# Optimization experiments

Measured on AMD Instinct MI355X. Metric: run time of the kernel, lower is better.

Reference implementation:

```python
import jax, jax.numpy as jnp
import numpy as np

V, F, H, P, C = 50000, 300, 256, 128, 10   # vocab, emb dim, n_hid, n_penultimate, n_class
B, S, N = 128, 16, 64                      # docs, sentences/doc, word nodes/sentence (last = master)
G, T = B * S, B * S * N                    # sentence graphs, total word nodes
EPS = 1e-5


def _mp(h, adj, w1, b1, w2, b2):
    # MessagePassing: neighborhood aggregation (block-diag spmm) + 2-layer ReLU MLP
    m = jnp.einsum('gij,gjf->gif', adj, h)
    return jax.nn.relu(jax.nn.relu(m @ w1 + b1) @ w2 + b2)


def _att(h, w, b, v, use_master):
    # Attention readout: alpha = softmax(relu(hW+b)v) over nodes, weighted sum;
    # with master node, last node is split off and concatenated to the pooled vector.
    if use_master:
        t, h = h[:, -1, :], h[:, :-1, :]
    logits = jnp.einsum('gnh,h->gn', jax.nn.relu(h @ w + b), v)
    alpha = jax.nn.softmax(logits, axis=1)
    pooled = jnp.einsum('gn,gnh->gh', alpha, h)
    return jnp.concatenate([pooled, t], axis=1) if use_master else pooled


def setup_inputs():
    key = jax.random.key(0)
    ks = iter(jax.random.split(key, 40))
    def nrm(shape, s=0.05):
        return jax.random.normal(next(ks), shape, jnp.float32) * s
    x = jax.random.randint(next(ks), (T,), 0, V)
    adj = jax.random.uniform(next(ks), (G, N, N), jnp.float32)
    adj = adj / jnp.sum(adj, -1, keepdims=True)         # row-normalized word-graph blocks
    adj_s = jax.random.uniform(next(ks), (B, S, S), jnp.float32)
    adj_s = adj_s / jnp.sum(adj_s, -1, keepdims=True)   # sentence-graph blocks (unused in sentence_att branch)
    return dict(
        x=x, adj=adj, adj_s=adj_s, shape0=N, shape1=S,
        emb=nrm((V, F), 0.1),
        mp0_w1=nrm((F, H)), mp0_b1=jnp.zeros((H,)), mp0_w2=nrm((H, H)), mp0_b2=jnp.zeros((H,)),
        mp1_w1=nrm((H, H)), mp1_b1=jnp.zeros((H,)), mp1_w2=nrm((H, H)), mp1_b2=jnp.zeros((H,)),
        att0_w=nrm((H, H)), att0_b=jnp.zeros((H,)), att0_v=nrm((H,)),
        att1_w=nrm((H, H)), att1_b=jnp.zeros((H,)), att1_v=nrm((H,)),
        bn_gamma=jnp.ones((4 * H,)), bn_beta=jnp.zeros((4 * H,)),
        fc1_w=nrm((4 * H, H)), fc1_b=jnp.zeros((H,)),
        satt_w=nrm((H, H)), satt_b=jnp.zeros((H,)), satt_v=nrm((H,)),
        fc2_w=nrm((H, P)), fc2_b=jnp.zeros((P,)),
        fc3_w=nrm((P, C)), fc3_b=jnp.zeros((C,)),
    )


def reference(x, adj, adj_s, shape0, shape1, emb,
              mp0_w1, mp0_b1, mp0_w2, mp0_b2,
              mp1_w1, mp1_b1, mp1_w2, mp1_b2,
              att0_w, att0_b, att0_v, att1_w, att1_b, att1_v,
              bn_gamma, bn_beta, fc1_w, fc1_b,
              satt_w, satt_b, satt_v, fc2_w, fc2_b, fc3_w, fc3_b):
    h = emb[x].reshape(-1, shape0, emb.shape[1])        # [G, N, F] (dropout is identity at eval)
    reps = []
    for (w1, b1, w2, b2, aw, ab, av) in (
            (mp0_w1, mp0_b1, mp0_w2, mp0_b2, att0_w, att0_b, att0_v),
            (mp1_w1, mp1_b1, mp1_w2, mp1_b2, att1_w, att1_b, att1_v)):
        h = _mp(h, adj, w1, b1, w2, b2)                  # [G, N, H]
        reps.append(_att(h, aw, ab, av, True))           # [G, 2H]
    z = jnp.concatenate(reps, axis=1)                    # [G, 2*n_mp*H] = [G, 4H]
    mu, var = jnp.mean(z, 0), jnp.var(z, 0)              # BatchNorm1d (batch statistics)
    z = (z - mu) / jnp.sqrt(var + EPS) * bn_gamma + bn_beta
    z = jax.nn.relu(z @ fc1_w + fc1_b)                   # [G, H]
    z = z.reshape(-1, shape1, z.shape[1])                # [B, S, H]
    z = _att(z, satt_w, satt_b, satt_v, False)           # sentence attention -> [B, H]
    z = jax.nn.relu(z @ fc2_w + fc2_b)                   # [B, P]
    z = z @ fc3_w + fc3_b                                # [B, C]
    return jax.nn.log_softmax(z, axis=1)
```

## Files before the change

kernel.cpp:

```cpp
#include <hip/hip_runtime.h>
#include <math.h>


typedef unsigned short u16;
typedef __attribute__((ext_vector_type(8))) short bf16x8;
typedef __attribute__((ext_vector_type(4))) float f32x4;

__device__ __forceinline__ float b2f(u16 v){ return __uint_as_float(((unsigned)v)<<16); }
__device__ __forceinline__ u16 f2b(float f){
    unsigned u = __float_as_uint(f);
    return (u16)((u + 0x7FFFu + ((u>>16)&1u)) >> 16);
}
__device__ __forceinline__ ushort4 pack4(float a,float b,float c,float d){
    ushort4 o; o.x=f2b(a); o.y=f2b(b); o.z=f2b(c); o.w=f2b(d); return o;
}

#define SCOL_OFF 32768
__device__ __forceinline__ int srow_b(int nd, int f){
    return (nd*512 + f*2) ^ ((nd&7)<<4);
}
__device__ __forceinline__ int scol_b(int f, int nd){
    return SCOL_OFF + ((f*128 + nd*2) ^ ((f&7)<<4));
}

__global__ __launch_bounds__(512, 2) void mega_k(
    const int* __restrict__ x, const u16* __restrict__ adjb,
    const u16* __restrict__ eprime,
    const u16* __restrict__ wb_w2a, const u16* __restrict__ wb_awa,
    const u16* __restrict__ wb_w1b, const u16* __restrict__ wb_w2b,
    const u16* __restrict__ wb_awb,
    const float* __restrict__ b1a, const float* __restrict__ b2a,
    const float* __restrict__ aba, const float* __restrict__ ava,
    const float* __restrict__ b1b, const float* __restrict__ b2b,
    const float* __restrict__ abb, const float* __restrict__ avb,
    u16* __restrict__ zb)
{
    __shared__ __align__(16) char sm[65536];
    const int g = blockIdx.x, tid = threadIdx.x;
    const int w = tid>>6, l = tid&63, lgp = l>>4, ll = l&15;
    const f32x4 zero4 = {0.f,0.f,0.f,0.f};

    {
        const int r2 = tid >> 3;
        const int fc = (tid & 7) * 32;
        const u16* ep = eprime + (long)x[g*64 + r2]*256 + fc;
        uint4 q0 = *(const uint4*)(ep);
        uint4 q1 = *(const uint4*)(ep + 8);
        uint4 q2 = *(const uint4*)(ep + 16);
        uint4 q3 = *(const uint4*)(ep + 24);
        #pragma unroll
        for (int qi=0; qi<4; ++qi){
            uint4 v = (qi==0)?q0:(qi==1)?q1:(qi==2)?q2:q3;
            unsigned xw[4] = {v.x, v.y, v.z, v.w};
            #pragma unroll
            for (int wi=0; wi<4; ++wi){
                unsigned u = xw[wi];
                int f0 = fc + qi*8 + wi*2;
                *(u16*)(sm + scol_b(f0,   r2)) = (u16)(u & 0xffffu);
                *(u16*)(sm + scol_b(f0+1, r2)) = (u16)(u >> 16);
            }
        }
        __syncthreads();
    }

    const u16* adjbg = adjb + (long)g*4096;

    #pragma unroll 1
    for (int layer=0; layer<2; ++layer){
        const u16* wb_w2 = layer ? wb_w2b : wb_w2a;
        const u16* wb_aw = layer ? wb_awb : wb_awa;
        const float* b1  = layer ? b1b : b1a;
        const float* b2  = layer ? b2b : b2a;
        const float* ab  = layer ? abb : aba;
        const float* av  = layer ? avb : ava;
        const int zoff   = layer ? 512 : 0;

        {
            f32x4 acc[2][4];
            #pragma unroll
            for (int j=0;j<4;++j){ acc[0][j] = zero4; acc[1][j] = zero4; }
            #pragma unroll
            for (int t=0;t<2;++t){
                const int k0 = t*32 + lgp*8;
                bf16x8 a0 = *(const bf16x8*)(sm + scol_b(w*32 +      ll, k0));
                bf16x8 a1 = *(const bf16x8*)(sm + scol_b(w*32 + 16 + ll, k0));
                bf16x8 b[4];
                #pragma unroll
                for (int ni=0;ni<4;++ni)
                    b[ni] = *(const bf16x8*)(adjbg + (ni*16+ll)*64 + k0);
                #pragma unroll
                for (int ni=0;ni<4;++ni){
                    acc[0][ni] = __builtin_amdgcn_mfma_f32_16x16x32_bf16(a0, b[ni], acc[0][ni],0,0,0);
                    acc[1][ni] = __builtin_amdgcn_mfma_f32_16x16x32_bf16(a1, b[ni], acc[1][ni],0,0,0);
                }
            }
            #pragma unroll
            for (int mi=0;mi<2;++mi){
                int f0 = w*32 + mi*16 + lgp*4;
                float4 bi = *(const float4*)(b1 + f0);
                #pragma unroll
                for (int ni=0;ni<4;++ni){
                    int nd = ni*16 + ll;
                    f32x4 v = acc[mi][ni];
                    *(ushort4*)(sm + srow_b(nd, f0)) = pack4(
                        fmaxf(v[0]+bi.x,0.f), fmaxf(v[1]+bi.y,0.f),
                        fmaxf(v[2]+bi.z,0.f), fmaxf(v[3]+bi.w,0.f));
                }
            }
            __syncthreads();
        }

        {
            f32x4 acc[2][4];
            #pragma unroll
            for (int j=0;j<4;++j){ acc[0][j] = zero4; acc[1][j] = zero4; }
            const u16* chw = wb_w2 + (w<<10) + ll*32 + lgp*8;
            bf16x8 w0 = *(const bf16x8*)(chw);
            bf16x8 w1 = *(const bf16x8*)(chw + 512);
            #pragma unroll
            for (int t=0;t<8;++t){
                bf16x8 cw0 = w0, cw1 = w1;
                if (t < 7){
                    const u16* nx = chw + (t+1)*8192;
                    w0 = *(const bf16x8*)(nx);
                    w1 = *(const bf16x8*)(nx + 512);
                }
                const int k0 = t*32 + lgp*8;
                bf16x8 b[4];
                #pragma unroll
                for (int ni=0;ni<4;++ni) b[ni] = *(const bf16x8*)(sm + srow_b(ni*16+ll, k0));
                #pragma unroll
                for (int ni=0;ni<4;++ni){
                    acc[0][ni] = __builtin_amdgcn_mfma_f32_16x16x32_bf16(cw0, b[ni], acc[0][ni],0,0,0);
                    acc[1][ni] = __builtin_amdgcn_mfma_f32_16x16x32_bf16(cw1, b[ni], acc[1][ni],0,0,0);
                }
            }
            __syncthreads();
            #pragma unroll
            for (int mi=0;mi<2;++mi){
                int f0 = w*32 + mi*16 + lgp*4;
                float4 bi = *(const float4*)(b2 + f0);
                #pragma unroll
                for (int ni=0;ni<4;++ni){
                    int nd = ni*16 + ll;
                    f32x4 v = acc[mi][ni];
                    *(ushort4*)(sm + srow_b(nd, f0)) = pack4(
                        fmaxf(v[0]+bi.x,0.f), fmaxf(v[1]+bi.y,0.f),
                        fmaxf(v[2]+bi.z,0.f), fmaxf(v[3]+bi.w,0.f));
                }
            }
            __syncthreads();
        }

        {
            f32x4 acc[4][2];
            #pragma unroll
            for (int i=0;i<4;++i){ acc[i][0] = zero4; acc[i][1] = zero4; }
            const u16* chw = wb_aw + (w<<10) + ll*32 + lgp*8;
            bf16x8 w0 = *(const bf16x8*)(chw);
            bf16x8 w1 = *(const bf16x8*)(chw + 512);
            #pragma unroll
            for (int t=0;t<8;++t){
                bf16x8 cw0 = w0, cw1 = w1;
                if (t < 7){
                    const u16* nx = chw + (t+1)*8192;
                    w0 = *(const bf16x8*)(nx);
                    w1 = *(const bf16x8*)(nx + 512);
                }
                const int k0 = t*32 + lgp*8;
                bf16x8 a[4];
                #pragma unroll
                for (int mi=0;mi<4;++mi) a[mi] = *(const bf16x8*)(sm + srow_b(mi*16+ll, k0));
                #pragma unroll
                for (int mi=0;mi<4;++mi){
                    acc[mi][0] = __builtin_amdgcn_mfma_f32_16x16x32_bf16(a[mi], cw0, acc[mi][0],0,0,0);
                    acc[mi][1] = __builtin_amdgcn_mfma_f32_16x16x32_bf16(a[mi], cw1, acc[mi][1],0,0,0);
                }
            }
            float abv[2], avv[2];
            #pragma unroll
            for (int ni=0;ni<2;++ni){ abv[ni] = ab[w*32+ni*16+ll]; avv[ni] = av[w*32+ni*16+ll]; }
            float lgt[4][4];
            #pragma unroll
            for (int mi=0;mi<4;++mi){
                #pragma unroll
                for (int r=0;r<4;++r) lgt[mi][r] = 0.f;
            }
            #pragma unroll
            for (int mi=0;mi<4;++mi){
                #pragma unroll
                for (int ni=0;ni<2;++ni){
                    f32x4 v = acc[mi][ni];
                    #pragma unroll
                    for (int r=0;r<4;++r) lgt[mi][r] += fmaxf(v[r]+abv[ni],0.f)*avv[ni];
                }
            }
            #pragma unroll
            for (int mi=0;mi<4;++mi){
                #pragma unroll
                for (int r=0;r<4;++r){
                    float vv = lgt[mi][r];
                    vv += __shfl_xor(vv,1,64); vv += __shfl_xor(vv,2,64);
                    vv += __shfl_xor(vv,4,64); vv += __shfl_xor(vv,8,64);
                    lgt[mi][r] = vv;
                }
            }
            float* red   = (float*)(sm + SCOL_OFF);
            float* alpha = (float*)(sm + SCOL_OFF + 2048);
            float* poolp = (float*)(sm + SCOL_OFF + 2304);
            if (ll == 0){
                #pragma unroll
                for (int mi=0;mi<4;++mi){
                    #pragma unroll
                    for (int r=0;r<4;++r){
                        int node = mi*16 + lgp*4 + r;
                        red[w*64 + node] = lgt[mi][r];
                    }
                }
            }
            __syncthreads();
            if (tid < 64){
                float lv = 0.f;
                #pragma unroll
                for (int ww=0;ww<8;++ww) lv += red[ww*64 + tid];
                float v = (tid < 63) ? lv : -INFINITY;
                float m = v;
                #pragma unroll
                for (int off=32; off; off>>=1) m = fmaxf(m, __shfl_xor(m, off, 64));
                float e = (tid < 63) ? expf(v - m) : 0.f;
                float s = e;
                #pragma unroll
                for (int off=32; off; off>>=1) s += __shfl_xor(s, off, 64);
                alpha[tid] = e / s;
            }
            __syncthreads();
            {
                const int c = tid & 255, half = tid >> 8;
                const int r0v = half ? 32 : 0, r1v = half ? 63 : 32;
                float pool = 0.f;
                for (int r=r0v; r<r1v; ++r)
                    pool += alpha[r]*b2f(*(const u16*)(sm + srow_b(r,c)));
                poolp[half*256 + c] = pool;
            }
            __syncthreads();
            if (tid < 256){
                const int c = tid;
                long zb0 = (long)g*1024 + zoff;
                zb[zb0 + c]       = f2b(poolp[c] + poolp[256+c]);
                zb[zb0 + 256 + c] = *(const u16*)(sm + srow_b(63,c));
            }
            __syncthreads();
        }

        if (layer == 0){
            f32x4 acc[4][2];
            #pragma unroll
            for (int i=0;i<4;++i){ acc[i][0] = zero4; acc[i][1] = zero4; }
            const u16* chw = wb_w1b + (w<<10) + ll*32 + lgp*8;
            bf16x8 w0 = *(const bf16x8*)(chw);
            bf16x8 w1 = *(const bf16x8*)(chw + 512);
            #pragma unroll
            for (int t=0;t<8;++t){
                bf16x8 cw0 = w0, cw1 = w1;
                if (t < 7){
                    const u16* nx = chw + (t+1)*8192;
                    w0 = *(const bf16x8*)(nx);
                    w1 = *(const bf16x8*)(nx + 512);
                }
                const int k0 = t*32 + lgp*8;
                bf16x8 a[4];
                #pragma unroll
                for (int mi=0;mi<4;++mi) a[mi] = *(const bf16x8*)(sm + srow_b(mi*16+ll, k0));
                #pragma unroll
                for (int mi=0;mi<4;++mi){
                    acc[mi][0] = __builtin_amdgcn_mfma_f32_16x16x32_bf16(a[mi], cw0, acc[mi][0],0,0,0);
                    acc[mi][1] = __builtin_amdgcn_mfma_f32_16x16x32_bf16(a[mi], cw1, acc[mi][1],0,0,0);
                }
            }
            __syncthreads();
            #pragma unroll
            for (int mi=0;mi<4;++mi){
                #pragma unroll
                for (int ni=0;ni<2;++ni){
                    int fo = w*32 + ni*16 + ll, nd0 = mi*16 + lgp*4;
                    f32x4 v = acc[mi][ni];
                    *(ushort4*)(sm + scol_b(fo,nd0)) = pack4(v[0],v[1],v[2],v[3]);
                }
            }
            __syncthreads();
        }
    }
}

__global__ __launch_bounds__(256) void eprime_k(
    const float* __restrict__ emb, const u16* __restrict__ blob,
    u16* __restrict__ eprime)
{
    __shared__ __align__(16) char sm[4096];
    const int h = blockIdx.x, m0 = blockIdx.y * 32;
    const int tid = threadIdx.x;
    const int w = tid>>6, l = tid&63, lgp = l>>4, ll = l&15;
    const f32x4 zero4 = {0.f,0.f,0.f,0.f};
    const int slab = h*4 + w;

    const int r  = tid >> 3;
    const int kc = (tid & 7) * 4;
    int rowg = m0 + r; if (rowg > 49999) rowg = 49999;
    const long arow = (long)rowg * 300;
    const int wbyte = (r*64 + (tid&7)*8) ^ ((r&7)<<4);

    float4 pv = (kc + 4 <= 300) ? *(const float4*)(emb + arow + kc)
                                : make_float4(0.f,0.f,0.f,0.f);
    const u16* chw = blob + (slab<<10) + ll*32 + lgp*8;
    bf16x8 w0 = *(const bf16x8*)(chw);
    bf16x8 w1 = *(const bf16x8*)(chw + 512);

    f32x4 acc[2][2];
    acc[0][0]=zero4; acc[0][1]=zero4; acc[1][0]=zero4; acc[1][1]=zero4;

    #pragma unroll
    for (int t=0;t<10;++t){
        float4 cur = pv;
        bf16x8 cw0 = w0, cw1 = w1;
        if (t < 9){
            int kn = (t+1)*32 + kc;
            pv = (kn + 4 <= 300) ? *(const float4*)(emb + arow + kn)
                                 : make_float4(0.f,0.f,0.f,0.f);
            const u16* nx = chw + (t+1)*8192;
            w0 = *(const bf16x8*)(nx);
            w1 = *(const bf16x8*)(nx + 512);
        }
        *(ushort4*)(sm + (t&1)*2048 + wbyte) = pack4(cur.x,cur.y,cur.z,cur.w);
        __syncthreads();
        const char* eb = sm + (t&1)*2048;
        bf16x8 a0, a1;
        {
            int row = ll;
            a0 = *(const bf16x8*)(eb + ((row*64 + lgp*16) ^ ((row&7)<<4)));
            row = 16 + ll;
            a1 = *(const bf16x8*)(eb + ((row*64 + lgp*16) ^ ((row&7)<<4)));
        }
        acc[0][0] = __builtin_amdgcn_mfma_f32_16x16x32_bf16(a0, cw0, acc[0][0],0,0,0);
        acc[0][1] = __builtin_amdgcn_mfma_f32_16x16x32_bf16(a0, cw1, acc[0][1],0,0,0);
        acc[1][0] = __builtin_amdgcn_mfma_f32_16x16x32_bf16(a1, cw0, acc[1][0],0,0,0);
        acc[1][1] = __builtin_amdgcn_mfma_f32_16x16x32_bf16(a1, cw1, acc[1][1],0,0,0);
        __syncthreads();
    }
    #pragma unroll
    for (int mi=0;mi<2;++mi){
        #pragma unroll
        for (int ni=0;ni<2;++ni){
            int col = h*128 + w*32 + ni*16 + ll;
            f32x4 v = acc[mi][ni];
            #pragma unroll
            for (int rr=0;rr<4;++rr){
                int row = m0 + mi*16 + lgp*4 + rr;
                if (row < 50000) eprime[(long)row*256 + col] = f2b(v[rr]);
            }
        }
    }
}

__global__ __launch_bounds__(256) void conv_all_k(
    const float* __restrict__ w1a, const float* __restrict__ w2a,
    const float* __restrict__ awa, const float* __restrict__ w1b,
    const float* __restrict__ w2b, const float* __restrict__ awb,
    u16* __restrict__ dst_base)
{
    long idx = (long)blockIdx.x*256 + threadIdx.x;
    if (idx >= 81920L + 5L*65536L) return;
    const float* src; u16* dst; int Ksrc; long rem;
    if (idx < 81920L){ src = w1a; dst = dst_base; Ksrc = 300; rem = idx; }
    else {
        long j = (idx - 81920L) / 65536L, r2 = (idx - 81920L) % 65536L;
        src = (j==0)?w2a:(j==1)?awa:(j==2)?w1b:(j==3)?w2b:awb;
        dst = dst_base + 81920L + j*65536L; Ksrc = 256; rem = r2;
    }
    int k = (int)(rem >> 8), n = (int)(rem & 255);
    float v = (k < Ksrc) ? src[k*256 + n] : 0.f;
    int t = k>>5, kk = k&31;
    dst[((t*8 + (n>>5))<<10) + (n&31)*32 + kk] = f2b(v);
}

__global__ __launch_bounds__(256) void adjconv_k(
    const float* __restrict__ adj, u16* __restrict__ adjb)
{
    long i = (long)blockIdx.x*256 + threadIdx.x;
    if (i < 2048L*4096L) adjb[i] = f2b(adj[i]);
}

__global__ __launch_bounds__(256) void bnstats_k(
    const u16* __restrict__ zb, const float* __restrict__ gamma,
    const float* __restrict__ beta,
    float* __restrict__ scale, float* __restrict__ shift)
{
    const int tid = threadIdx.x;
    const int cl = tid & 3, ph = tid >> 2;
    const int c = blockIdx.x * 4 + cl;
    double s = 0.0, s2 = 0.0;
    #pragma unroll 8
    for (int r = ph; r < 2048; r += 64) {
        float v = b2f(zb[(long)r * 1024 + c]);
        s += v; s2 += (double)v * v;
    }
    __shared__ double ss[256], ss2[256];
    ss[tid] = s; ss2[tid] = s2;
    __syncthreads();
    for (int off = 128; off >= 4; off >>= 1){
        if (tid < off){ ss[tid] += ss[tid+off]; ss2[tid] += ss2[tid+off]; }
        __syncthreads();
    }
    if (tid < 4){
        int cc = blockIdx.x * 4 + tid;
        double mu = ss[tid] / 2048.0;
        double var = ss2[tid] / 2048.0 - mu * mu;
        float inv = (float)(1.0 / sqrt(var + 1e-5));
        float sc = gamma[cc] * inv;
        scale[cc] = sc;
        shift[cc] = beta[cc] - (float)mu * sc;
    }
}

__global__ __launch_bounds__(256) void wconv_fc1_k(
    const float* __restrict__ fw, const float* __restrict__ scale,
    u16* __restrict__ dst)
{
    int lin = blockIdx.x*256 + threadIdx.x;
    int c = lin >> 10, t = c >> 3, s = c & 7;
    int nl = (lin >> 5) & 31, kk = lin & 31;
    int n = s*32 + nl, k = t*32 + kk;
    dst[lin] = f2b(fw[k*256 + n] * scale[k]);
}

__global__ __launch_bounds__(256) void fusefc1_k(
    const float* __restrict__ fw, const float* __restrict__ shift,
    const float* __restrict__ fb, float* __restrict__ biasp)
{
    const int n = blockIdx.x, tid = threadIdx.x;
    float p = 0.f;
    #pragma unroll
    for (int i=0;i<4;++i){
        int k = tid + i*256;
        p += shift[k] * fw[k*256 + n];
    }
    __shared__ float red[256];
    red[tid] = p;
    __syncthreads();
    for (int off=128; off; off>>=1){
        if (tid < off) red[tid] += red[tid+off];
        __syncthreads();
    }
    if (tid == 0) biasp[n] = fb[n] + red[0];
}

__global__ __launch_bounds__(256) void fc1_mfma_k(
    const u16* __restrict__ zb, const u16* __restrict__ blob,
    const float* __restrict__ biasp, float* __restrict__ z2)
{
    __shared__ __align__(16) char sm[4096];
    const int h = blockIdx.x, m0 = blockIdx.y * 32;
    const int tid = threadIdx.x;
    const int w = tid>>6, l = tid&63, lgp = l>>4, ll = l&15;
    const f32x4 zero4 = {0.f,0.f,0.f,0.f};
    const int slab = h*4 + w;

    const int r  = tid >> 3;
    const int kc = (tid & 7) * 4;
    const long arow = (long)(m0 + r) * 1024;
    const int wbyte = (r*64 + (tid&7)*8) ^ ((r&7)<<4);

    ushort4 pv = *(const ushort4*)(zb + arow + kc);
    const u16* chw = blob + (slab<<10) + ll*32 + lgp*8;
    bf16x8 w0 = *(const bf16x8*)(chw);
    bf16x8 w1 = *(const bf16x8*)(chw + 512);

    f32x4 acc[2][2];
    acc[0][0]=zero4; acc[0][1]=zero4; acc[1][0]=zero4; acc[1][1]=zero4;

    #pragma unroll 4
    for (int t=0;t<32;++t){
        ushort4 cur = pv;
        bf16x8 cw0 = w0, cw1 = w1;
        if (t < 31){
            pv = *(const ushort4*)(zb + arow + (t+1)*32 + kc);
            const u16* nx = chw + (t+1)*8192;
            w0 = *(const bf16x8*)(nx);
            w1 = *(const bf16x8*)(nx + 512);
        }
        *(ushort4*)(sm + (t&1)*2048 + wbyte) = cur;
        __syncthreads();
        const char* eb = sm + (t&1)*2048;
        bf16x8 a0, a1;
        {
            int row = ll;
            a0 = *(const bf16x8*)(eb + ((row*64 + lgp*16) ^ ((row&7)<<4)));
            row = 16 + ll;
            a1 = *(const bf16x8*)(eb + ((row*64 + lgp*16) ^ ((row&7)<<4)));
        }
        acc[0][0] = __builtin_amdgcn_mfma_f32_16x16x32_bf16(a0, cw0, acc[0][0],0,0,0);
        acc[0][1] = __builtin_amdgcn_mfma_f32_16x16x32_bf16(a0, cw1, acc[0][1],0,0,0);
        acc[1][0] = __builtin_amdgcn_mfma_f32_16x16x32_bf16(a1, cw0, acc[1][0],0,0,0);
        acc[1][1] = __builtin_amdgcn_mfma_f32_16x16x32_bf16(a1, cw1, acc[1][1],0,0,0);
        __syncthreads();
    }
    #pragma unroll
    for (int mi=0;mi<2;++mi){
        #pragma unroll
        for (int ni=0;ni<2;++ni){
            int col = h*128 + w*32 + ni*16 + ll;
            float bv = biasp[col];
            f32x4 v = acc[mi][ni];
            #pragma unroll
            for (int rr=0;rr<4;++rr){
                int row = m0 + mi*16 + lgp*4 + rr;
                z2[(long)row*256 + col] = fmaxf(v[rr] + bv, 0.f);
            }
        }
    }
}

__global__ __launch_bounds__(256) void sattfinal_k(
    const float* __restrict__ z2, const float* __restrict__ sw,
    const float* __restrict__ sb, const float* __restrict__ sv,
    const float* __restrict__ w2, const float* __restrict__ b2,
    const float* __restrict__ w3, const float* __restrict__ b3,
    float* __restrict__ out)
{
    const int b = blockIdx.x;
    const int tid = threadIdx.x;
    __shared__ float zs[16][256];
    for (int idx = tid; idx < 16 * 256; idx += 256) {
        int r = idx >> 8, c = idx & 255;
        zs[r][c] = z2[((long)b * 16 + r) * 256 + c];
    }
    __syncthreads();

    float acc[16] = {};
    for (int k = 0; k < 256; ++k) {
        float w = sw[k * 256 + tid];
        #pragma unroll
        for (int r = 0; r < 16; ++r) acc[r] += zs[r][k] * w;
    }
    const float sbv = sb[tid], svv = sv[tid];

    __shared__ float red[16][4];
    __shared__ float logit_s[16], alpha_s[16];
    const int warp = tid >> 6, lane = tid & 63;
    #pragma unroll
    for (int r = 0; r < 16; ++r) {
        float u = fmaxf(acc[r] + sbv, 0.f);
        float lv = u * svv;
        #pragma unroll
        for (int off = 32; off; off >>= 1) lv += __shfl_down(lv, off, 64);
        if (lane == 0) red[r][warp] = lv;
    }
    __syncthreads();
    if (tid < 16) logit_s[tid] = red[tid][0] + red[tid][1] + red[tid][2] + red[tid][3];
    __syncthreads();
    if (tid < 16) {
        float m = -INFINITY;
        #pragma unroll
        for (int i = 0; i < 16; ++i) m = fmaxf(m, logit_s[i]);
        float ssum = 0.f;
        #pragma unroll
        for (int i = 0; i < 16; ++i) ssum += expf(logit_s[i] - m);
        alpha_s[tid] = expf(logit_s[tid] - m) / ssum;
    }
    __syncthreads();
    float pacc = 0.f;
    #pragma unroll
    for (int r = 0; r < 16; ++r) pacc += alpha_s[r] * zs[r][tid];

    __shared__ float ps[256], z3s[128], z4s[10];
    ps[tid] = pacc;
    __syncthreads();
    if (tid < 128){
        float a2 = b2[tid];
        for (int k = 0; k < 256; ++k) a2 += ps[k] * w2[k * 128 + tid];
        z3s[tid] = fmaxf(a2, 0.f);
    }
    __syncthreads();
    if (tid < 10){
        float a3 = b3[tid];
        for (int k = 0; k < 128; ++k) a3 += z3s[k] * w3[k * 10 + tid];
        z4s[tid] = a3;
    }
    __syncthreads();
    if (tid < 10){
        float m = z4s[0];
        #pragma unroll
        for (int i = 1; i < 10; ++i) m = fmaxf(m, z4s[i]);
        float s = 0.f;
        #pragma unroll
        for (int i = 0; i < 10; ++i) s += expf(z4s[i] - m);
        out[b * 10 + tid] = z4s[tid] - m - logf(s);
    }
}

extern "C" void kernel_launch(void* const* d_in, const int* in_sizes, int n_in,
                              void* d_out, int out_size, void* d_ws, size_t ws_size,
                              hipStream_t stream)
{
    const int*   x      = (const int*)d_in[0];
    const float* adj    = (const float*)d_in[1];
    const float* emb    = (const float*)d_in[5];
    const float* mp0_w1 = (const float*)d_in[6];
    const float* mp0_b1 = (const float*)d_in[7];
    const float* mp0_w2 = (const float*)d_in[8];
    const float* mp0_b2 = (const float*)d_in[9];
    const float* mp1_w1 = (const float*)d_in[10];
    const float* mp1_b1 = (const float*)d_in[11];
    const float* mp1_w2 = (const float*)d_in[12];
    const float* mp1_b2 = (const float*)d_in[13];
    const float* att0_w = (const float*)d_in[14];
    const float* att0_b = (const float*)d_in[15];
    const float* att0_v = (const float*)d_in[16];
    const float* att1_w = (const float*)d_in[17];
    const float* att1_b = (const float*)d_in[18];
    const float* att1_v = (const float*)d_in[19];
    const float* bn_g   = (const float*)d_in[20];
    const float* bn_b   = (const float*)d_in[21];
    const float* fc1_w  = (const float*)d_in[22];
    const float* fc1_b  = (const float*)d_in[23];
    const float* satt_w = (const float*)d_in[24];
    const float* satt_b = (const float*)d_in[25];
    const float* satt_v = (const float*)d_in[26];
    const float* fc2_w  = (const float*)d_in[27];
    const float* fc2_b  = (const float*)d_in[28];
    const float* fc3_w  = (const float*)d_in[29];
    const float* fc3_b  = (const float*)d_in[30];
    float* out = (float*)d_out;

    float* ws = (float*)d_ws;
    float* z2      = ws;
    float* scale   = z2 + 2048L * 256;
    float* shiftv  = scale + 1024;
    float* biasp   = shiftv + 1024;
    u16*   wbase   = (u16*)(biasp + 256);
    u16* wb_w1a  = wbase;
    u16* wb_w2a  = wb_w1a + 81920;
    u16* wb_awa  = wb_w2a + 65536;
    u16* wb_w1b  = wb_awa + 65536;
    u16* wb_w2b  = wb_w1b + 65536;
    u16* wb_awb  = wb_w2b + 65536;
    u16* adjb    = wb_awb + 65536;
    u16* zb      = adjb + 2048L*4096;
    u16* fc1blob = zb + 2048L*1024;
    u16* eprime  = fc1blob + 262144;

    conv_all_k<<<dim3(1600), dim3(256), 0, stream>>>(
        mp0_w1, mp0_w2, att0_w, mp1_w1, mp1_w2, att1_w, wbase);
    adjconv_k<<<dim3(32768), dim3(256), 0, stream>>>(adj, adjb);
    eprime_k<<<dim3(2, 1563), dim3(256), 0, stream>>>(emb, wb_w1a, eprime);

    mega_k<<<dim3(2048), dim3(512), 0, stream>>>(
        x, adjb, eprime,
        wb_w2a, wb_awa, wb_w1b, wb_w2b, wb_awb,
        mp0_b1, mp0_b2, att0_b, att0_v,
        mp1_b1, mp1_b2, att1_b, att1_v, zb);

    bnstats_k<<<dim3(256), dim3(256), 0, stream>>>(zb, bn_g, bn_b, scale, shiftv);
    wconv_fc1_k<<<dim3(1024), dim3(256), 0, stream>>>(fc1_w, scale, fc1blob);
    fusefc1_k<<<dim3(256), dim3(256), 0, stream>>>(fc1_w, shiftv, fc1_b, biasp);
    fc1_mfma_k<<<dim3(2, 64), dim3(256), 0, stream>>>(zb, fc1blob, biasp, z2);
    sattfinal_k<<<dim3(128), dim3(256), 0, stream>>>(z2, satt_w, satt_b, satt_v,
        fc2_w, fc2_b, fc3_w, fc3_b, out);
}
```

Measured before the change: 328.6 us.

## Process two sentence graphs per block with 4 warps each and larger per-warp tiles

The fused message-passing kernel now handles two graphs per 512-thread block, each on its own 64KB shared-memory half. Each group of four warps computes a 64x64 output tile instead of 32x64, so every weight fragment loaded from global memory feeds twice as many MFMAs and weight traffic per graph drops. The attention softmax and pooling reductions are reorganised per half, which removes one barrier stage. In exchange, shared memory doubles to 128KB and each thread holds more accumulator registers, which may limit blocks per CU and reduce latency hiding.

Result: faster. 319.9 us (-2.7%).

```diff
diff --git a/kernel.cpp b/kernel.cpp
--- a/kernel.cpp
+++ b/kernel.cpp
@@ -21,6 +21,9 @@
 }
 __device__ __forceinline__ int scol_b(int f, int nd){
     return SCOL_OFF + ((f*128 + nd*2) ^ ((f&7)<<4));
+}
+__device__ __forceinline__ int wfrag_off(int ni){
+    return ((ni>>1)<<10) + ((ni&1)<<9);
 }
 
 __global__ __launch_bounds__(512, 2) void mega_k(
@@ -35,35 +38,42 @@
     const float* __restrict__ abb, const float* __restrict__ avb,
     u16* __restrict__ zb)
 {
-    __shared__ __align__(16) char sm[65536];
-    const int g = blockIdx.x, tid = threadIdx.x;
+    __shared__ __align__(16) char sm[131072];
+    const int tid = threadIdx.x;
     const int w = tid>>6, l = tid&63, lgp = l>>4, ll = l&15;
+    const int q = w>>2, w4 = w&3, slab = w4*64;
+    const long g = (long)blockIdx.x*2 + q;
+    char* smq = sm + q*65536;
     const f32x4 zero4 = {0.f,0.f,0.f,0.f};
 
     {
         const int r2 = tid >> 3;
         const int fc = (tid & 7) * 32;
-        const u16* ep = eprime + (long)x[g*64 + r2]*256 + fc;
-        uint4 q0 = *(const uint4*)(ep);
-        uint4 q1 = *(const uint4*)(ep + 8);
-        uint4 q2 = *(const uint4*)(ep + 16);
-        uint4 q3 = *(const uint4*)(ep + 24);
-        #pragma unroll
-        for (int qi=0; qi<4; ++qi){
-            uint4 v = (qi==0)?q0:(qi==1)?q1:(qi==2)?q2:q3;
-            unsigned xw[4] = {v.x, v.y, v.z, v.w};
-            #pragma unroll
-            for (int wi=0; wi<4; ++wi){
-                unsigned u = xw[wi];
-                int f0 = fc + qi*8 + wi*2;
-                *(u16*)(sm + scol_b(f0,   r2)) = (u16)(u & 0xffffu);
-                *(u16*)(sm + scol_b(f0+1, r2)) = (u16)(u >> 16);
+        #pragma unroll
+        for (int q2=0; q2<2; ++q2){
+            const u16* ep = eprime + (long)x[((long)blockIdx.x*2+q2)*64 + r2]*256 + fc;
+            char* smr = sm + q2*65536;
+            uint4 qa = *(const uint4*)(ep);
+            uint4 qb = *(const uint4*)(ep + 8);
+            uint4 qc = *(const uint4*)(ep + 16);
+            uint4 qd = *(const uint4*)(ep + 24);
+            #pragma unroll
+            for (int qi=0; qi<4; ++qi){
+                uint4 v = (qi==0)?qa:(qi==1)?qb:(qi==2)?qc:qd;
+                unsigned xw[4] = {v.x, v.y, v.z, v.w};
+                #pragma unroll
+                for (int wi=0; wi<4; ++wi){
+                    unsigned u = xw[wi];
+                    int f0 = fc + qi*8 + wi*2;
+                    *(u16*)(smr + scol_b(f0,   r2)) = (u16)(u & 0xffffu);
+                    *(u16*)(smr + scol_b(f0+1, r2)) = (u16)(u >> 16);
+                }
             }
         }
         __syncthreads();
     }
 
-    const u16* adjbg = adjb + (long)g*4096;
+    const u16* adjg = adjb + g*4096;
 
     #pragma unroll 1
     for (int layer=0; layer<2; ++layer){
@@ -76,33 +86,38 @@
         const int zoff   = layer ? 512 : 0;
 
         {
-            f32x4 acc[2][4];
-            #pragma unroll
-            for (int j=0;j<4;++j){ acc[0][j] = zero4; acc[1][j] = zero4; }
+            f32x4 acc[4][4];
+            #pragma unroll
+            for (int i=0;i<4;++i){
+                #pragma unroll
+                for (int j=0;j<4;++j) acc[i][j] = zero4;
+            }
             #pragma unroll
             for (int t=0;t<2;++t){
                 const int k0 = t*32 + lgp*8;
-                bf16x8 a0 = *(const bf16x8*)(sm + scol_b(w*32 +      ll, k0));
-                bf16x8 a1 = *(const bf16x8*)(sm + scol_b(w*32 + 16 + ll, k0));
-                bf16x8 b[4];
+                bf16x8 a[4], b[4];
+                #pragma unroll
+                for (int mi=0;mi<4;++mi)
+                    a[mi] = *(const bf16x8*)(smq + scol_b(slab + mi*16 + ll, k0));
                 #pragma unroll
                 for (int ni=0;ni<4;++ni)
-                    b[ni] = *(const bf16x8*)(adjbg + (ni*16+ll)*64 + k0);
-                #pragma unroll
-                for (int ni=0;ni<4;++ni){
-                    acc[0][ni] = __builtin_amdgcn_mfma_f32_16x16x32_bf16(a0, b[ni], acc[0][ni],0,0,0);
-                    acc[1][ni] = __builtin_amdgcn_mfma_f32_16x16x32_bf16(a1, b[ni], acc[1][ni],0,0,0);
-                }
-            }
-            #pragma unroll
-            for (int mi=0;mi<2;++mi){
-                int f0 = w*32 + mi*16 + lgp*4;
+                    b[ni] = *(const bf16x8*)(adjg + (ni*16+ll)*64 + k0);
+                #pragma unroll
+                for (int mi=0;mi<4;++mi){
+                    #pragma unroll
+                    for (int ni=0;ni<4;++ni)
+                        acc[mi][ni] = __builtin_amdgcn_mfma_f32_16x16x32_bf16(a[mi], b[ni], acc[mi][ni],0,0,0);
+                }
+            }
+            #pragma unroll
+            for (int mi=0;mi<4;++mi){
+                int f0 = slab + mi*16 + lgp*4;
                 float4 bi = *(const float4*)(b1 + f0);
                 #pragma unroll
                 for (int ni=0;ni<4;++ni){
                     int nd = ni*16 + ll;
                     f32x4 v = acc[mi][ni];
-                    *(ushort4*)(sm + srow_b(nd, f0)) = pack4(
+                    *(ushort4*)(smq + srow_b(nd, f0)) = pack4(
                         fmaxf(v[0]+bi.x,0.f), fmaxf(v[1]+bi.y,0.f),
                         fmaxf(v[2]+bi.z,0.f), fmaxf(v[3]+bi.w,0.f));
                 }
@@ -111,40 +126,48 @@
         }
 
         {
-            f32x4 acc[2][4];
-            #pragma unroll
-            for (int j=0;j<4;++j){ acc[0][j] = zero4; acc[1][j] = zero4; }
-            const u16* chw = wb_w2 + (w<<10) + ll*32 + lgp*8;
-            bf16x8 w0 = *(const bf16x8*)(chw);
-            bf16x8 w1 = *(const bf16x8*)(chw + 512);
+            f32x4 acc[4][4];
+            #pragma unroll
+            for (int i=0;i<4;++i){
+                #pragma unroll
+                for (int j=0;j<4;++j) acc[i][j] = zero4;
+            }
+            const u16* chw = wb_w2 + ((w4*2)<<10) + ll*32 + lgp*8;
+            bf16x8 cw[4], nw[4];
+            #pragma unroll
+            for (int ni=0;ni<4;++ni) cw[ni] = *(const bf16x8*)(chw + wfrag_off(ni));
             #pragma unroll
             for (int t=0;t<8;++t){
-                bf16x8 cw0 = w0, cw1 = w1;
                 if (t < 7){
-                    const u16* nx = chw + (t+1)*8192;
-                    w0 = *(const bf16x8*)(nx);
-                    w1 = *(const bf16x8*)(nx + 512);
+                    #pragma unroll
+                    for (int ni=0;ni<4;++ni)
+                        nw[ni] = *(const bf16x8*)(chw + (t+1)*8192 + wfrag_off(ni));
                 }
                 const int k0 = t*32 + lgp*8;
                 bf16x8 b[4];
                 #pragma unroll
-                for (int ni=0;ni<4;++ni) b[ni] = *(const bf16x8*)(sm + srow_b(ni*16+ll, k0));
-                #pragma unroll
-                for (int ni=0;ni<4;++ni){
-                    acc[0][ni] = __builtin_amdgcn_mfma_f32_16x16x32_bf16(cw0, b[ni], acc[0][ni],0,0,0);
-                    acc[1][ni] = __builtin_amdgcn_mfma_f32_16x16x32_bf16(cw1, b[ni], acc[1][ni],0,0,0);
+                for (int ni=0;ni<4;++ni) b[ni] = *(const bf16x8*)(smq + srow_b(ni*16+ll, k0));
+                #pragma unroll
+                for (int mi=0;mi<4;++mi){
+                    #pragma unroll
+                    for (int ni=0;ni<4;++ni)
+                        acc[mi][ni] = __builtin_amdgcn_mfma_f32_16x16x32_bf16(cw[mi], b[ni], acc[mi][ni],0,0,0);
+                }
+                if (t < 7){
+                    #pragma unroll
+                    for (int ni=0;ni<4;++ni) cw[ni] = nw[ni];
                 }
             }
             __syncthreads();
             #pragma unroll
-            for (int mi=0;mi<2;++mi){
-                int f0 = w*32 + mi*16 + lgp*4;
+            for (int mi=0;mi<4;++mi){
+                int f0 = slab + mi*16 + lgp*4;
                 float4 bi = *(const float4*)(b2 + f0);
                 #pragma unroll
                 for (int ni=0;ni<4;++ni){
                     int nd = ni*16 + ll;
                     f32x4 v = acc[mi][ni];
-                    *(ushort4*)(sm + srow_b(nd, f0)) = pack4(
+                    *(ushort4*)(smq + srow_b(nd, f0)) = pack4(
                         fmaxf(v[0]+bi.x,0.f), fmaxf(v[1]+bi.y,0.f),
                         fmaxf(v[2]+bi.z,0.f), fmaxf(v[3]+bi.w,0.f));
                 }
@@ -153,33 +176,44 @@
         }
 
         {
-            f32x4 acc[4][2];
-            #pragma unroll
-            for (int i=0;i<4;++i){ acc[i][0] = zero4; acc[i][1] = zero4; }
-            const u16* chw = wb_aw + (w<<10) + ll*32 + lgp*8;
-            bf16x8 w0 = *(const bf16x8*)(chw);
-            bf16x8 w1 = *(const bf16x8*)(chw + 512);
+            f32x4 acc[4][4];
+            #pragma unroll
+            for (int i=0;i<4;++i){
+                #pragma unroll
+                for (int j=0;j<4;++j) acc[i][j] = zero4;
+            }
+            const u16* chw = wb_aw + ((w4*2)<<10) + ll*32 + lgp*8;
+            bf16x8 cw[4], nw[4];
+            #pragma unroll
+            for (int ni=0;ni<4;++ni) cw[ni] = *(const bf16x8*)(chw + wfrag_off(ni));
             #pragma unroll
             for (int t=0;t<8;++t){
-                bf16x8 cw0 = w0, cw1 = w1;
                 if (t < 7){
-                    const u16* nx = chw + (t+1)*8192;
-                    w0 = *(const bf16x8*)(nx);
-                    w1 = *(const bf16x8*)(nx + 512);
+                    #pragma unroll
+                    for (int ni=0;ni<4;++ni)
+                        nw[ni] = *(const bf16x8*)(chw + (t+1)*8192 + wfrag_off(ni));
                 }
                 const int k0 = t*32 + lgp*8;
                 bf16x8 a[4];
                 #pragma unroll
-                for (int mi=0;mi<4;++mi) a[mi] = *(const bf16x8*)(sm + srow_b(mi*16+ll, k0));
+                for (int mi=0;mi<4;++mi) a[mi] = *(const bf16x8*)(smq + srow_b(mi*16+ll, k0));
                 #pragma unroll
                 for (int mi=0;mi<4;++mi){
-                    acc[mi][0] = __builtin_amdgcn_mfma_f32_16x16x32_bf16(a[mi], cw0, acc[mi][0],0,0,0);
-                    acc[mi][1] = __builtin_amdgcn_mfma_f32_16x16x32_bf16(a[mi], cw1, acc[mi][1],0,0,0);
-                }
-            }
-            float abv[2], avv[2];
-            #pragma unroll
-            for (int ni=0;ni<2;++ni){ abv[ni] = ab[w*32+ni*16+ll]; avv[ni] = av[w*32+ni*16+ll]; }
+                    #pragma unroll
+                    for (int ni=0;ni<4;++ni)
+                        acc[mi][ni] = __builtin_amdgcn_mfma_f32_16x16x32_bf16(a[mi], cw[ni], acc[mi][ni],0,0,0);
+                }
+                if (t < 7){
+                    #pragma unroll
+                    for (int ni=0;ni<4;++ni) cw[ni] = nw[ni];
+                }
+            }
+            float abv[4], avv[4];
+            #pragma unroll
+            for (int ni=0;ni<4;++ni){
+                int c = slab + ni*16 + ll;
+                abv[ni] = ab[c]; avv[ni] = av[c];
+            }
             float lgt[4][4];
             #pragma unroll
             for (int mi=0;mi<4;++mi){
@@ -189,7 +223,7 @@
             #pragma unroll
             for (int mi=0;mi<4;++mi){
                 #pragma unroll
-                for (int ni=0;ni<2;++ni){
+                for (int ni=0;ni<4;++ni){
                     f32x4 v = acc[mi][ni];
                     #pragma unroll
                     for (int r=0;r<4;++r) lgt[mi][r] += fmaxf(v[r]+abv[ni],0.f)*avv[ni];
@@ -205,86 +239,88 @@
                     lgt[mi][r] = vv;
                 }
             }
-            float* red   = (float*)(sm + SCOL_OFF);
-            float* alpha = (float*)(sm + SCOL_OFF + 2048);
-            float* poolp = (float*)(sm + SCOL_OFF + 2304);
+            float* red = (float*)(smq + SCOL_OFF);
             if (ll == 0){
                 #pragma unroll
                 for (int mi=0;mi<4;++mi){
                     #pragma unroll
                     for (int r=0;r<4;++r){
                         int node = mi*16 + lgp*4 + r;
-                        red[w*64 + node] = lgt[mi][r];
+                        red[w4*64 + node] = lgt[mi][r];
                     }
                 }
             }
             __syncthreads();
-            if (tid < 64){
-                float lv = 0.f;
-                #pragma unroll
-                for (int ww=0;ww<8;++ww) lv += red[ww*64 + tid];
-                float v = (tid < 63) ? lv : -INFINITY;
+            if (tid < 128){
+                int qs = tid >> 6, t64 = tid & 63;
+                const float* rq = (const float*)(sm + qs*65536 + SCOL_OFF);
+                float lv = rq[t64] + rq[64+t64] + rq[128+t64] + rq[192+t64];
+                float v = (t64 < 63) ? lv : -INFINITY;
                 float m = v;
                 #pragma unroll
                 for (int off=32; off; off>>=1) m = fmaxf(m, __shfl_xor(m, off, 64));
-                float e = (tid < 63) ? expf(v - m) : 0.f;
+                float e = (t64 < 63) ? expf(v - m) : 0.f;
                 float s = e;
                 #pragma unroll
                 for (int off=32; off; off>>=1) s += __shfl_xor(s, off, 64);
-                alpha[tid] = e / s;
+                *(float*)(sm + qs*65536 + SCOL_OFF + 1024 + t64*4) = e / s;
             }
             __syncthreads();
             {
-                const int c = tid & 255, half = tid >> 8;
-                const int r0v = half ? 32 : 0, r1v = half ? 63 : 32;
+                int qs = tid >> 8, c = tid & 255;
+                char* smr = sm + qs*65536;
+                const float* alpha = (const float*)(smr + SCOL_OFF + 1024);
                 float pool = 0.f;
-                for (int r=r0v; r<r1v; ++r)
-                    pool += alpha[r]*b2f(*(const u16*)(sm + srow_b(r,c)));
-                poolp[half*256 + c] = pool;
+                for (int r=0;r<63;++r)
+                    pool += alpha[r]*b2f(*(const u16*)(smr + srow_b(r,c)));
+                long zb0 = ((long)blockIdx.x*2 + qs)*1024 + zoff;
+                zb[zb0 + c]       = f2b(pool);
+                zb[zb0 + 256 + c] = *(const u16*)(smr + srow_b(63,c));
             }
             __syncthreads();
-            if (tid < 256){
-                const int c = tid;
-                long zb0 = (long)g*1024 + zoff;
-                zb[zb0 + c]       = f2b(poolp[c] + poolp[256+c]);
-                zb[zb0 + 256 + c] = *(const u16*)(sm + srow_b(63,c));
-            }
-            __syncthreads();
         }
 
         if (layer == 0){
-            f32x4 acc[4][2];
-            #pragma unroll
-            for (int i=0;i<4;++i){ acc[i][0] = zero4; acc[i][1] = zero4; }
-            const u16* chw = wb_w1b + (w<<10) + ll*32 + lgp*8;
-            bf16x8 w0 = *(const bf16x8*)(chw);
-            bf16x8 w1 = *(const bf16x8*)(chw + 512);
+            f32x4 acc[4][4];
+            #pragma unroll
+            for (int i=0;i<4;++i){
+                #pragma unroll
+                for (int j=0;j<4;++j) acc[i][j] = zero4;
+            }
+            const u16* chw = wb_w1b + ((w4*2)<<10) + ll*32 + lgp*8;
+            bf16x8 cw[4], nw[4];
+            #pragma unroll
+            for (int ni=0;ni<4;++ni) cw[ni] = *(const bf16x8*)(chw + wfrag_off(ni));
             #pragma unroll
             for (int t=0;t<8;++t){
-                bf16x8 cw0 = w0, cw1 = w1;
                 if (t < 7){
-                    const u16* nx = chw + (t+1)*8192;
-                    w0 = *(const bf16x8*)(nx);
-                    w1 = *(const bf16x8*)(nx + 512);
+                    #pragma unroll
+                    for (int ni=0;ni<4;++ni)
+                        nw[ni] = *(const bf16x8*)(chw + (t+1)*8192 + wfrag_off(ni));
                 }
                 const int k0 = t*32 + lgp*8;
                 bf16x8 a[4];
                 #pragma unroll
-                for (int mi=0;mi<4;++mi) a[mi] = *(const bf16x8*)(sm + srow_b(mi*16+ll, k0));
+                for (int mi=0;mi<4;++mi) a[mi] = *(const bf16x8*)(smq + srow_b(mi*16+ll, k0));
                 #pragma unroll
                 for (int mi=0;mi<4;++mi){
-                    acc[mi][0] = __builtin_amdgcn_mfma_f32_16x16x32_bf16(a[mi], cw0, acc[mi][0],0,0,0);
-                    acc[mi][1] = __builtin_amdgcn_mfma_f32_16x16x32_bf16(a[mi], cw1, acc[mi][1],0,0,0);
+                    #pragma unroll
+                    for (int ni=0;ni<4;++ni)
+                        acc[mi][ni] = __builtin_amdgcn_mfma_f32_16x16x32_bf16(a[mi], cw[ni], acc[mi][ni],0,0,0);
+                }
+                if (t < 7){
+                    #pragma unroll
+                    for (int ni=0;ni<4;++ni) cw[ni] = nw[ni];
                 }
             }
             __syncthreads();
             #pragma unroll
             for (int mi=0;mi<4;++mi){
                 #pragma unroll
-                for (int ni=0;ni<2;++ni){
-                    int fo = w*32 + ni*16 + ll, nd0 = mi*16 + lgp*4;
+                for (int ni=0;ni<4;++ni){
+                    int fo = slab + ni*16 + ll, nd0 = mi*16 + lgp*4;
                     f32x4 v = acc[mi][ni];
-                    *(ushort4*)(sm + scol_b(fo,nd0)) = pack4(v[0],v[1],v[2],v[3]);
+                    *(ushort4*)(smq + scol_b(fo,nd0)) = pack4(v[0],v[1],v[2],v[3]);
                 }
             }
             __syncthreads();
@@ -653,7 +689,7 @@
     adjconv_k<<<dim3(32768), dim3(256), 0, stream>>>(adj, adjb);
     eprime_k<<<dim3(2, 1563), dim3(256), 0, stream>>>(emb, wb_w1a, eprime);
 
-    mega_k<<<dim3(2048), dim3(512), 0, stream>>>(
+    mega_k<<<dim3(1024), dim3(512), 0, stream>>>(
         x, adjb, eprime,
         wb_w2a, wb_awa, wb_w1b, wb_w2b, wb_awb,
         mp0_b1, mp0_b2, att0_b, att0_v,
```
